# Kernel optimization log

Measured on AMD Instinct MI355X. Metric: run time of the kernel, lower is better.

Reference implementation:

```python
import jax, jax.numpy as jnp
import numpy as np

N_NODES = 200000
N_EDGES = 6400000
N_GRAPHS = 512
DIM_IN = 128
HID = 32
BN_EPS = 1e-5


def _gin(x, src, dst, w1, b1, w2, b2):
    # GINConv with eps=0: MLP(x + sum_{j in N(i)} x_j)
    agg = jax.ops.segment_sum(x[src], dst, num_segments=N_NODES)
    h = x + agg
    h = jnp.maximum(h @ w1 + b1, 0.0)
    return h @ w2 + b2


def _bn(x, gamma, beta):
    # BatchNorm1d, training mode: batch stats, biased variance
    m = jnp.mean(x, axis=0)
    v = jnp.var(x, axis=0)
    return gamma * (x - m) * jax.lax.rsqrt(v + BN_EPS) + beta


def setup_inputs() -> dict:
    key = jax.random.key(0)
    ks = jax.random.split(key, 20)
    s = 0.1
    inp = {
        "x": jax.random.normal(ks[0], (N_NODES, DIM_IN), jnp.float32),
        "edge_index": jax.random.randint(ks[1], (2, N_EDGES), 0, N_NODES, jnp.int32),
        "batch": jnp.sort(jax.random.randint(ks[2], (N_NODES,), 0, N_GRAPHS, jnp.int32)),
        "e0_w1": s * jax.random.normal(ks[3], (DIM_IN, HID), jnp.float32),
        "e0_b1": s * jax.random.normal(ks[4], (HID,), jnp.float32),
        "e0_w2": s * jax.random.normal(ks[5], (HID, HID), jnp.float32),
        "e0_b2": s * jax.random.normal(ks[6], (HID,), jnp.float32),
        "enc_w1": s * jax.random.normal(ks[7], (4, HID, HID), jnp.float32),
        "enc_b1": s * jax.random.normal(ks[8], (4, HID), jnp.float32),
        "enc_w2": s * jax.random.normal(ks[9], (4, HID, HID), jnp.float32),
        "enc_b2": s * jax.random.normal(ks[10], (4, HID), jnp.float32),
        "enc_gamma": jnp.ones((5, HID), jnp.float32),
        "enc_beta": jnp.zeros((5, HID), jnp.float32),
        "dec_w1": s * jax.random.normal(ks[11], (5, HID, HID), jnp.float32),
        "dec_b1": s * jax.random.normal(ks[12], (5, HID), jnp.float32),
        "dec_w2": s * jax.random.normal(ks[13], (4, HID, HID), jnp.float32),
        "dec_b2": s * jax.random.normal(ks[14], (4, HID), jnp.float32),
        "dec_w2_last": s * jax.random.normal(ks[15], (HID, DIM_IN), jnp.float32),
        "dec_b2_last": s * jax.random.normal(ks[16], (DIM_IN,), jnp.float32),
        "dec_gamma": jnp.ones((4, HID), jnp.float32),
        "dec_beta": jnp.zeros((4, HID), jnp.float32),
    }
    return inp


def reference(x, edge_index, batch,
              e0_w1, e0_b1, e0_w2, e0_b2,
              enc_w1, enc_b1, enc_w2, enc_b2, enc_gamma, enc_beta,
              dec_w1, dec_b1, dec_w2, dec_b2, dec_w2_last, dec_b2_last,
              dec_gamma, dec_beta):
    src, dst = edge_index[0], edge_index[1]

    # ----- Encoder: 5 GIN layers, ReLU then BN, collect per-layer reps -----
    xs = []
    h = jnp.maximum(_gin(x, src, dst, e0_w1, e0_b1, e0_w2, e0_b2), 0.0)
    h = _bn(h, enc_gamma[0], enc_beta[0])
    xs.append(h)
    for i in range(4):
        h = jnp.maximum(_gin(h, src, dst, enc_w1[i], enc_b1[i], enc_w2[i], enc_b2[i]), 0.0)
        h = _bn(h, enc_gamma[i + 1], enc_beta[i + 1])
        xs.append(h)
    encoded_rep = h

    # ----- Decoder: 5 GIN layers, ReLU; BN on all but last -----
    d = encoded_rep
    for i in range(5):
        w2 = dec_w2[i] if i < 4 else dec_w2_last
        b2 = dec_b2[i] if i < 4 else dec_b2_last
        d = jnp.maximum(_gin(d, src, dst, dec_w1[i], dec_b1[i], w2, b2), 0.0)
        if i < 4:
            d = _bn(d, dec_gamma[i], dec_beta[i])
    decoded_rep = d

    # ----- Global add pool of each encoder layer output, concat -----
    xpool = [jax.ops.segment_sum(xi, batch, num_segments=N_GRAPHS) for xi in xs]
    global_rep = jnp.concatenate(xpool, axis=1)  # [G, 5*32]

    return encoded_rep, decoded_rep, global_rep
```

## Files before the change

kernel.cpp:

```cpp
#include <hip/hip_runtime.h>
#include <hip/hip_bf16.h>
#include <hip/hip_fp16.h>
#include <string.h>

#define N_NODES  200000
#define N_EDGES  6400000
#define N_GRAPHS 512
#define DIM_IN   128
#define HID      32
#define BN_EPS   1e-5f

#define CHUNK    2048
#define NCHUNKS  98

typedef const float* fp;

__device__ __forceinline__ unsigned short f2h(float f) {
    __half h = __float2half(f);
    unsigned short u; __builtin_memcpy(&u, &h, 2); return u;
}
__device__ __forceinline__ float2 h2f2(unsigned int u) {
    __half2 h; __builtin_memcpy(&h, &u, 4);
    return __half22float2(h);
}
__device__ __forceinline__ float h1f(unsigned short u) {
    __half h; __builtin_memcpy(&h, &u, 2);
    return __half2float(h);
}


__global__ __launch_bounds__(256) void k_hist2(const int* __restrict__ dst,
                                               int* __restrict__ deg) {
    __shared__ int lh[12500];
    const int grp = blockIdx.x & 15;
    const int blk = blockIdx.x >> 4;
    const int lo = grp * 12500;
    for (int j = threadIdx.x; j < 12500; j += 256) lh[j] = 0;
    __syncthreads();
    const int4* d4 = reinterpret_cast<const int4*>(dst) + blk * 50000;
    for (int j = threadIdx.x; j < 12500; j += 256) {
        int4 v0 = d4[j];
        int4 v1 = d4[j + 12500];
        int4 v2 = d4[j + 25000];
        int4 v3 = d4[j + 37500];
        int a;
        a = v0.x - lo; if ((unsigned)a < 12500u) atomicAdd(&lh[a], 1);
        a = v0.y - lo; if ((unsigned)a < 12500u) atomicAdd(&lh[a], 1);
        a = v0.z - lo; if ((unsigned)a < 12500u) atomicAdd(&lh[a], 1);
        a = v0.w - lo; if ((unsigned)a < 12500u) atomicAdd(&lh[a], 1);
        a = v1.x - lo; if ((unsigned)a < 12500u) atomicAdd(&lh[a], 1);
        a = v1.y - lo; if ((unsigned)a < 12500u) atomicAdd(&lh[a], 1);
        a = v1.z - lo; if ((unsigned)a < 12500u) atomicAdd(&lh[a], 1);
        a = v1.w - lo; if ((unsigned)a < 12500u) atomicAdd(&lh[a], 1);
        a = v2.x - lo; if ((unsigned)a < 12500u) atomicAdd(&lh[a], 1);
        a = v2.y - lo; if ((unsigned)a < 12500u) atomicAdd(&lh[a], 1);
        a = v2.z - lo; if ((unsigned)a < 12500u) atomicAdd(&lh[a], 1);
        a = v2.w - lo; if ((unsigned)a < 12500u) atomicAdd(&lh[a], 1);
        a = v3.x - lo; if ((unsigned)a < 12500u) atomicAdd(&lh[a], 1);
        a = v3.y - lo; if ((unsigned)a < 12500u) atomicAdd(&lh[a], 1);
        a = v3.z - lo; if ((unsigned)a < 12500u) atomicAdd(&lh[a], 1);
        a = v3.w - lo; if ((unsigned)a < 12500u) atomicAdd(&lh[a], 1);
    }
    __syncthreads();
    for (int j = threadIdx.x; j < 12500; j += 256) {
        int c = lh[j];
        if (c) atomicAdd(&deg[lo + j], c);
    }
}

__global__ void k_chunksum(const int* __restrict__ deg, int* __restrict__ chunksum) {
    __shared__ int red[256];
    int b = blockIdx.x, t = threadIdx.x;
    int base = b * CHUNK;
    int s = 0;
    for (int k = 0; k < 8; ++k) {
        int i = base + t + k * 256;
        if (i < N_NODES) s += deg[i];
    }
    red[t] = s; __syncthreads();
    for (int off = 128; off > 0; off >>= 1) {
        if (t < off) red[t] += red[t + off];
        __syncthreads();
    }
    if (t == 0) chunksum[b] = red[0];
}

__global__ void k_scanchunks(const int* __restrict__ chunksum, int* __restrict__ chunkoff,
                             int* __restrict__ rowptr) {
    __shared__ int buf[128];
    int t = threadIdx.x;
    int v = (t < NCHUNKS) ? chunksum[t] : 0;
    buf[t] = v; __syncthreads();
    for (int off = 1; off < 128; off <<= 1) {
        int add = (t >= off) ? buf[t - off] : 0;
        __syncthreads();
        buf[t] += add;
        __syncthreads();
    }
    if (t < NCHUNKS) chunkoff[t] = buf[t] - v;
    if (t == 0) rowptr[N_NODES] = N_EDGES;
}

__global__ void k_scanfinal(const int* __restrict__ deg, const int* __restrict__ chunkoff,
                            int* __restrict__ rowptr, int* __restrict__ fillpos) {
    __shared__ int tsum[256];
    int b = blockIdx.x, t = threadIdx.x;
    int base = b * CHUNK + t * 8;
    int v[8]; int s = 0;
    for (int k = 0; k < 8; ++k) {
        int i = base + k;
        v[k] = (i < N_NODES) ? deg[i] : 0;
        s += v[k];
    }
    tsum[t] = s; __syncthreads();
    for (int off = 1; off < 256; off <<= 1) {
        int add = (t >= off) ? tsum[t - off] : 0;
        __syncthreads();
        tsum[t] += add;
        __syncthreads();
    }
    int run = tsum[t] - s + chunkoff[b];
    for (int k = 0; k < 8; ++k) {
        int i = base + k;
        if (i < N_NODES) { rowptr[i] = run; fillpos[i] = run; run += v[k]; }
    }
}

__global__ __launch_bounds__(256) void k_fill2(
    const int* __restrict__ src, const int* __restrict__ dst,
    int* __restrict__ fillpos, int* __restrict__ csr, int blk0)
{
    const int grp = blockIdx.x & 7;
    const int blk = blk0 + (blockIdx.x >> 3);
    const int lo = grp * 25000, hi = lo + 25000;
    const int4* d4 = reinterpret_cast<const int4*>(dst) + blk * 3125;
    const int4* s4 = reinterpret_cast<const int4*>(src) + blk * 3125;
    for (int j = threadIdx.x; j < 3125; j += 256) {
        int4 d = d4[j];
        int4 s = s4[j];
        if (d.x >= lo && d.x < hi) { int p = atomicAdd(&fillpos[d.x], 1); csr[p] = s.x; }
        if (d.y >= lo && d.y < hi) { int p = atomicAdd(&fillpos[d.y], 1); csr[p] = s.y; }
        if (d.z >= lo && d.z < hi) { int p = atomicAdd(&fillpos[d.z], 1); csr[p] = s.z; }
        if (d.w >= lo && d.w < hi) { int p = atomicAdd(&fillpos[d.w], 1); csr[p] = s.w; }
    }
}

__global__ void k_bounds(const int* __restrict__ batch, int* __restrict__ gstart) {
    int g = blockIdx.x * blockDim.x + threadIdx.x;
    if (g > N_GRAPHS) return;
    if (g == N_GRAPHS) { gstart[g] = N_NODES; return; }
    int lo = 0, hi = N_NODES;
    while (lo < hi) {
        int mid = (lo + hi) >> 1;
        if (batch[mid] < g) lo = mid + 1; else hi = mid;
    }
    gstart[g] = lo;
}


__global__ __launch_bounds__(256) void k_proj128(
    const float* __restrict__ x, fp w1,
    unsigned short* __restrict__ y16, int n0, int n1)
{
    const int lane = threadIdx.x & 63;
    const int c = lane & 31;
    const int kb = (lane & 32) * 2;
    const int srcBase = lane & 32;
    float wreg[64];
    #pragma unroll
    for (int k = 0; k < 64; ++k) wreg[k] = w1[(kb + k) * 32 + c];
    int worker   = (blockIdx.x * blockDim.x + threadIdx.x) >> 6;
    int nworkers = (gridDim.x * blockDim.x) >> 6;
    for (int n = n0 + 2 * worker; n < n1; n += 2 * nworkers) {
        const float* xa = x + (size_t)n * DIM_IN;
        const float* xb = xa + DIM_IN;
        float a02 = xa[kb + c], a13 = xa[kb + 32 + c];
        float b02 = xb[kb + c], b13 = xb[kb + 32 + c];
        float accA0 = 0.f, accA1 = 0.f, accB0 = 0.f, accB1 = 0.f;
        #pragma unroll
        for (int k = 0; k < 32; ++k) {
            float xav0 = __shfl(a02, srcBase | k, 64);
            float xav1 = __shfl(a13, srcBase | k, 64);
            float xbv0 = __shfl(b02, srcBase | k, 64);
            float xbv1 = __shfl(b13, srcBase | k, 64);
            accA0 = fmaf(xav0, wreg[k],      accA0);
            accA1 = fmaf(xav1, wreg[32 + k], accA1);
            accB0 = fmaf(xbv0, wreg[k],      accB0);
            accB1 = fmaf(xbv1, wreg[32 + k], accB1);
        }
        float accA = accA0 + accA1;
        float accB = accB0 + accB1;
        accA += __shfl_xor(accA, 32, 64);
        accB += __shfl_xor(accB, 32, 64);
        if (srcBase == 0) {
            y16[(size_t)n * 32 + c] = f2h(accA);
            y16[(size_t)(n + 1) * 32 + c] = f2h(accB);
        }
    }
}


__global__ __launch_bounds__(256) void k_gather8(
    const unsigned short* __restrict__ h16,
    const int* __restrict__ rowptr, const int* __restrict__ csr,
    float* __restrict__ sout,
    const float* __restrict__ stats, fp gamma, fp beta)
{
    const int lane = threadIdx.x & 63;
    const int sub  = lane & 15;
    const int q    = sub & 7;
    const int hh   = sub >> 3;
    const int srcBase = lane & 48;
    float sc0 = 1.f, sc1 = 1.f, sc2 = 1.f, sc3 = 1.f;
    float sh0 = 0.f, sh1 = 0.f, sh2 = 0.f, sh3 = 0.f;
    if (stats) {
        const int c0 = 4 * q;
        float m0 = stats[c0 + 0] * (1.f / N_NODES);
        float m1 = stats[c0 + 1] * (1.f / N_NODES);
        float m2 = stats[c0 + 2] * (1.f / N_NODES);
        float m3 = stats[c0 + 3] * (1.f / N_NODES);
        float v0 = stats[32 + c0 + 0] * (1.f / N_NODES) - m0 * m0;
        float v1 = stats[32 + c0 + 1] * (1.f / N_NODES) - m1 * m1;
        float v2 = stats[32 + c0 + 2] * (1.f / N_NODES) - m2 * m2;
        float v3 = stats[32 + c0 + 3] * (1.f / N_NODES) - m3 * m3;
        sc0 = gamma[c0 + 0] * rsqrtf(v0 + BN_EPS);
        sc1 = gamma[c0 + 1] * rsqrtf(v1 + BN_EPS);
        sc2 = gamma[c0 + 2] * rsqrtf(v2 + BN_EPS);
        sc3 = gamma[c0 + 3] * rsqrtf(v3 + BN_EPS);
        sh0 = beta[c0 + 0] - m0 * sc0;
        sh1 = beta[c0 + 1] - m1 * sc1;
        sh2 = beta[c0 + 2] - m2 * sc2;
        sh3 = beta[c0 + 3] - m3 * sc3;
    }
    const uint2* hp2 = reinterpret_cast<const uint2*>(h16);
    float4* so4 = reinterpret_cast<float4*>(sout);
    int worker   = (blockIdx.x * blockDim.x + threadIdx.x) >> 4;
    int nworkers = (gridDim.x * blockDim.x) >> 4;
    for (int n = worker; n < N_NODES; n += nworkers) {
        uint2 us = hp2[(size_t)n * 8 + q];
        int e0 = rowptr[n], e1 = rowptr[n + 1];
        float2 sA = h2f2(us.x), sB = h2f2(us.y);
        float a0 = (hh == 0) ? sA.x : 0.f;
        float a1 = (hh == 0) ? sA.y : 0.f;
        float a2 = (hh == 0) ? sB.x : 0.f;
        float a3 = (hh == 0) ? sB.y : 0.f;
        int e = e0;
        while (e < e1) {
            int rem = e1 - e;
            int cnt = rem < 16 ? rem : 16;
            int myidx = (sub < cnt) ? csr[e + sub] : 0;
            if (cnt == 16) {
                int i0 = __shfl(myidx, srcBase | (0  + hh), 64);
                int i1 = __shfl(myidx, srcBase | (2  + hh), 64);
                int i2 = __shfl(myidx, srcBase | (4  + hh), 64);
                int i3 = __shfl(myidx, srcBase | (6  + hh), 64);
                int i4 = __shfl(myidx, srcBase | (8  + hh), 64);
                int i5 = __shfl(myidx, srcBase | (10 + hh), 64);
                int i6 = __shfl(myidx, srcBase | (12 + hh), 64);
                int i7 = __shfl(myidx, srcBase | (14 + hh), 64);
                uint2 u0 = hp2[(size_t)i0 * 8 + q];
                uint2 u1 = hp2[(size_t)i1 * 8 + q];
                uint2 u2 = hp2[(size_t)i2 * 8 + q];
                uint2 u3 = hp2[(size_t)i3 * 8 + q];
                uint2 u4 = hp2[(size_t)i4 * 8 + q];
                uint2 u5 = hp2[(size_t)i5 * 8 + q];
                uint2 u6 = hp2[(size_t)i6 * 8 + q];
                uint2 u7 = hp2[(size_t)i7 * 8 + q];
                float2 fA, fB;
                fA = h2f2(u0.x); fB = h2f2(u0.y);
                a0 += fA.x; a1 += fA.y; a2 += fB.x; a3 += fB.y;
                fA = h2f2(u1.x); fB = h2f2(u1.y);
                a0 += fA.x; a1 += fA.y; a2 += fB.x; a3 += fB.y;
                fA = h2f2(u2.x); fB = h2f2(u2.y);
                a0 += fA.x; a1 += fA.y; a2 += fB.x; a3 += fB.y;
                fA = h2f2(u3.x); fB = h2f2(u3.y);
                a0 += fA.x; a1 += fA.y; a2 += fB.x; a3 += fB.y;
                fA = h2f2(u4.x); fB = h2f2(u4.y);
                a0 += fA.x; a1 += fA.y; a2 += fB.x; a3 += fB.y;
                fA = h2f2(u5.x); fB = h2f2(u5.y);
                a0 += fA.x; a1 += fA.y; a2 += fB.x; a3 += fB.y;
                fA = h2f2(u6.x); fB = h2f2(u6.y);
                a0 += fA.x; a1 += fA.y; a2 += fB.x; a3 += fB.y;
                fA = h2f2(u7.x); fB = h2f2(u7.y);
                a0 += fA.x; a1 += fA.y; a2 += fB.x; a3 += fB.y;
            } else {
                int k = 0;
                for (; k + 2 <= cnt; k += 2) {
                    int i = __shfl(myidx, srcBase | (k + hh), 64);
                    uint2 u = hp2[(size_t)i * 8 + q];
                    float2 fA = h2f2(u.x), fB = h2f2(u.y);
                    a0 += fA.x; a1 += fA.y; a2 += fB.x; a3 += fB.y;
                }
                if (k < cnt) {
                    int i = __shfl(myidx, srcBase | k, 64);
                    if (hh == 0) {
                        uint2 u = hp2[(size_t)i * 8 + q];
                        float2 fA = h2f2(u.x), fB = h2f2(u.y);
                        a0 += fA.x; a1 += fA.y; a2 += fB.x; a3 += fB.y;
                    }
                }
            }
            e += cnt;
        }
        a0 += __shfl_xor(a0, 8, 64);
        a1 += __shfl_xor(a1, 8, 64);
        a2 += __shfl_xor(a2, 8, 64);
        a3 += __shfl_xor(a3, 8, 64);
        float dc = (float)(e1 - e0 + 1);
        float4 o;
        o.x = fmaf(a0, sc0, dc * sh0);
        o.y = fmaf(a1, sc1, dc * sh1);
        o.z = fmaf(a2, sc2, dc * sh2);
        o.w = fmaf(a3, sc3, dc * sh3);
        if (hh == 0) so4[(size_t)n * 8 + q] = o;
    }
}


__global__ __launch_bounds__(256) void k_mlp32(
    const float* __restrict__ s, fp w1, fp b1, fp w2, fp b2,
    unsigned short* __restrict__ h16out,
    float* __restrict__ stats)
{
    const int lane = threadIdx.x & 63;
    const int c = lane & 31;
    const int srcBase = lane & 32;
    float w1r[32], w2r[32];
    #pragma unroll
    for (int k = 0; k < 32; ++k) {
        w1r[k] = w1[k * 32 + c];
        w2r[k] = w2[k * 32 + c];
    }
    const float b1c = b1[c];
    const float b2c = b2[c];
    int worker   = (blockIdx.x * blockDim.x + threadIdx.x) >> 5;
    int nworkers = (gridDim.x * blockDim.x) >> 5;
    float s1 = 0.f, s2 = 0.f;
    for (int n = worker; n < N_NODES; n += nworkers) {
        float sv = s[(size_t)n * 32 + c];
        float acc1 = b1c;
        #pragma unroll
        for (int k = 0; k < 32; ++k)
            acc1 = fmaf(__shfl(sv, srcBase | k, 64), w1r[k], acc1);
        float h3 = fmaxf(acc1, 0.f);
        float acc2 = b2c;
        #pragma unroll
        for (int k = 0; k < 32; ++k)
            acc2 = fmaf(__shfl(h3, srcBase | k, 64), w2r[k], acc2);
        float a = fmaxf(acc2, 0.f);
        h16out[(size_t)n * 32 + c] = f2h(a);
        s1 += a; s2 += a * a;
    }
    s1 += __shfl_xor(s1, 32, 64);
    s2 += __shfl_xor(s2, 32, 64);
    __shared__ float ls1[4][32], ls2[4][32];
    int w = threadIdx.x >> 6;
    if ((threadIdx.x & 32) == 0) { ls1[w][c] = s1; ls2[w][c] = s2; }
    __syncthreads();
    if (threadIdx.x < 32) {
        float t1 = ls1[0][c] + ls1[1][c] + ls1[2][c] + ls1[3][c];
        float t2 = ls2[0][c] + ls2[1][c] + ls2[2][c] + ls2[3][c];
        atomicAdd(&stats[c], t1);
        atomicAdd(&stats[32 + c], t2);
    }
}

__global__ __launch_bounds__(256) void k_mlp0(
    const float* __restrict__ s, fp b1, fp w2, fp b2,
    unsigned short* __restrict__ h16out,
    float* __restrict__ stats)
{
    const int lane = threadIdx.x & 63;
    const int c = lane & 31;
    const int srcBase = lane & 32;
    float w2r[32];
    #pragma unroll
    for (int k = 0; k < 32; ++k) w2r[k] = w2[k * 32 + c];
    const float b1c = b1[c];
    const float b2c = b2[c];
    int worker   = (blockIdx.x * blockDim.x + threadIdx.x) >> 5;
    int nworkers = (gridDim.x * blockDim.x) >> 5;
    float s1 = 0.f, s2 = 0.f;
    for (int n = worker; n < N_NODES; n += nworkers) {
        float sv = s[(size_t)n * 32 + c];
        float h3 = fmaxf(sv + b1c, 0.f);
        float acc2 = b2c;
        #pragma unroll
        for (int k = 0; k < 32; ++k)
            acc2 = fmaf(__shfl(h3, srcBase | k, 64), w2r[k], acc2);
        float a = fmaxf(acc2, 0.f);
        h16out[(size_t)n * 32 + c] = f2h(a);
        s1 += a; s2 += a * a;
    }
    s1 += __shfl_xor(s1, 32, 64);
    s2 += __shfl_xor(s2, 32, 64);
    __shared__ float ls1[4][32], ls2[4][32];
    int w = threadIdx.x >> 6;
    if ((threadIdx.x & 32) == 0) { ls1[w][c] = s1; ls2[w][c] = s2; }
    __syncthreads();
    if (threadIdx.x < 32) {
        float t1 = ls1[0][c] + ls1[1][c] + ls1[2][c] + ls1[3][c];
        float t2 = ls2[0][c] + ls2[1][c] + ls2[2][c] + ls2[3][c];
        atomicAdd(&stats[c], t1);
        atomicAdd(&stats[32 + c], t2);
    }
}

__global__ __launch_bounds__(256) void k_mlp_last(
    const float* __restrict__ s, fp w1, fp b1, fp w2 , fp b2,
    float* __restrict__ out, int n0, int n1)
{
    const int lane = threadIdx.x & 63;
    const int c = lane & 31;
    float w1r[32], w2a[32], w2b[32];
    #pragma unroll
    for (int k = 0; k < 32; ++k) {
        w1r[k] = w1[k * 32 + c];
        w2a[k] = w2[k * 128 + 2 * lane];
        w2b[k] = w2[k * 128 + 2 * lane + 1];
    }
    const float b1c = b1[c];
    const float b2a = b2[2 * lane];
    const float b2b = b2[2 * lane + 1];
    int worker   = (blockIdx.x * blockDim.x + threadIdx.x) >> 6;
    int nworkers = (gridDim.x * blockDim.x) >> 6;
    for (int n = n0 + 2 * worker; n < n1; n += 2 * nworkers) {
        float svA = s[(size_t)n * 32 + c];
        float svB = s[(size_t)(n + 1) * 32 + c];
        float p0A = b1c, p1A = 0.f, p0B = b1c, p1B = 0.f;
        #pragma unroll
        for (int k = 0; k < 16; ++k) {
            p0A = fmaf(__shfl(svA, k, 64),      w1r[k],      p0A);
            p1A = fmaf(__shfl(svA, 16 + k, 64), w1r[16 + k], p1A);
            p0B = fmaf(__shfl(svB, k, 64),      w1r[k],      p0B);
            p1B = fmaf(__shfl(svB, 16 + k, 64), w1r[16 + k], p1B);
        }
        float h3A = fmaxf(p0A + p1A, 0.f);
        float h3B = fmaxf(p0B + p1B, 0.f);
        float oaA = b2a, obA = b2b, oaB = b2a, obB = b2b;
        #pragma unroll
        for (int k = 0; k < 32; ++k) {
            float vA = __shfl(h3A, (lane & 32) | k, 64);
            float vB = __shfl(h3B, (lane & 32) | k, 64);
            oaA = fmaf(vA, w2a[k], oaA);
            obA = fmaf(vA, w2b[k], obA);
            oaB = fmaf(vB, w2a[k], oaB);
            obB = fmaf(vB, w2b[k], obB);
        }
        float2 prA; prA.x = fmaxf(oaA, 0.f); prA.y = fmaxf(obA, 0.f);
        float2 prB; prB.x = fmaxf(oaB, 0.f); prB.y = fmaxf(obB, 0.f);
        reinterpret_cast<float2*>(out)[(size_t)n * 64 + lane] = prA;
        reinterpret_cast<float2*>(out)[(size_t)(n + 1) * 64 + lane] = prB;
    }
}

__global__ void k_bnout(const unsigned short* __restrict__ h16,
                        const float* __restrict__ stats,
                        fp gamma, fp beta, float* __restrict__ out)
{
    const int c0 = (threadIdx.x & 15) * 2;
    float m0  = stats[c0] * (1.f / N_NODES);
    float m1  = stats[c0 + 1] * (1.f / N_NODES);
    float v0 = stats[32 + c0] * (1.f / N_NODES) - m0 * m0;
    float v1 = stats[32 + c0 + 1] * (1.f / N_NODES) - m1 * m1;
    float sc0 = gamma[c0] * rsqrtf(v0 + BN_EPS);
    float sc1 = gamma[c0 + 1] * rsqrtf(v1 + BN_EPS);
    float sh0 = beta[c0] - m0 * sc0;
    float sh1 = beta[c0 + 1] - m1 * sc1;
    const unsigned int* hp = reinterpret_cast<const unsigned int*>(h16);
    float2* o2 = reinterpret_cast<float2*>(out);
    int i = blockIdx.x * blockDim.x + threadIdx.x;
    int stride = gridDim.x * blockDim.x;
    for (; i < N_NODES * 16; i += stride) {
        float2 f = h2f2(hp[i]);
        float2 o;
        o.x = fmaf(f.x, sc0, sh0);
        o.y = fmaf(f.y, sc1, sh1);
        o2[i] = o;
    }
}

__global__ void k_pool(const unsigned short* __restrict__ h16,
                       const int* __restrict__ gstart,
                       float* __restrict__ out, int col0,
                       const float* __restrict__ stats, fp gamma, fp beta)
{
    int g = blockIdx.x;
    int t = threadIdx.x;
    int f = t & 31, j = t >> 5;
    int n0 = gstart[g], n1 = gstart[g + 1];
    float s = 0.f;
    for (int n = n0 + j; n < n1; n += 8) s += h1f(h16[(size_t)n * 32 + f]);
    __shared__ float red[8][32];
    red[j][f] = s; __syncthreads();
    if (t < 32) {
        float tot = 0.f;
        #pragma unroll
        for (int k = 0; k < 8; ++k) tot += red[k][f];
        float m  = stats[f] * (1.f / N_NODES);
        float vv = stats[32 + f] * (1.f / N_NODES) - m * m;
        float sc = gamma[f] * rsqrtf(vv + BN_EPS);
        float sh = beta[f] - m * sc;
        out[g * (5 * HID) + col0 + f] = fmaf(tot, sc, (float)(n1 - n0) * sh);
    }
}


extern "C" void kernel_launch(void* const* d_in, const int* in_sizes, int n_in,
                              void* d_out, int out_size, void* d_ws, size_t ws_size,
                              hipStream_t stream) {
    fp         x        = (fp)d_in[0];
    const int* edge     = (const int*)d_in[1];
    const int* batch    = (const int*)d_in[2];
    fp e0_w1 = (fp)d_in[3],  e0_b1 = (fp)d_in[4];
    fp e0_w2 = (fp)d_in[5],  e0_b2 = (fp)d_in[6];
    fp enc_w1 = (fp)d_in[7],  enc_b1 = (fp)d_in[8];
    fp enc_w2 = (fp)d_in[9],  enc_b2 = (fp)d_in[10];
    fp enc_gamma = (fp)d_in[11], enc_beta = (fp)d_in[12];
    fp dec_w1 = (fp)d_in[13], dec_b1 = (fp)d_in[14];
    fp dec_w2 = (fp)d_in[15], dec_b2 = (fp)d_in[16];
    fp dec_w2_last = (fp)d_in[17], dec_b2_last = (fp)d_in[18];
    fp dec_gamma = (fp)d_in[19], dec_beta = (fp)d_in[20];

    const int* srcp = edge;
    const int* dstp = edge + N_EDGES;

    float* out_enc    = (float*)d_out;
    float* out_dec    = (float*)d_out + (size_t)N_NODES * 32;
    float* out_global = (float*)d_out + (size_t)N_NODES * 160;

    char* p = (char*)d_ws;
    auto alloc = [&](size_t bytes) -> void* {
        void* r = (void*)p;
        p += (bytes + 255) & ~(size_t)255;
        return r;
    };
    int*   rowptr   = (int*)alloc((N_NODES + 1) * sizeof(int));
    int*   fillpos  = (int*)alloc(N_NODES * sizeof(int));
    int*   deg      = (int*)alloc(N_NODES * sizeof(int));
    int*   chunksum = (int*)alloc(128 * sizeof(int));
    int*   chunkoff = (int*)alloc(128 * sizeof(int));
    int*   gstart   = (int*)alloc((N_GRAPHS + 1) * sizeof(int));
    float* stats    = (float*)alloc(9 * 64 * sizeof(float));
    int*   csr      = (int*)alloc((size_t)N_EDGES * sizeof(int));
    float* sbuf     = (float*)alloc((size_t)N_NODES * 32 * sizeof(float));
    unsigned short* h16 = (unsigned short*)alloc((size_t)N_NODES * 32 * sizeof(unsigned short));

    hipMemsetAsync(deg, 0, N_NODES * sizeof(int), stream);
    hipMemsetAsync(stats, 0, 9 * 64 * sizeof(float), stream);

    k_hist2<<<512, 256, 0, stream>>>(dstp, deg);
    k_chunksum<<<NCHUNKS, 256, 0, stream>>>(deg, chunksum);
    k_scanchunks<<<1, 128, 0, stream>>>(chunksum, chunkoff, rowptr);
    k_scanfinal<<<NCHUNKS, 256, 0, stream>>>(deg, chunkoff, rowptr, fillpos);
    k_fill2<<<1368, 256, 0, stream>>>(srcp, dstp, fillpos, csr, 0);
    k_fill2<<<1368, 256, 0, stream>>>(srcp, dstp, fillpos, csr, 171);
    k_fill2<<<1360, 256, 0, stream>>>(srcp, dstp, fillpos, csr, 342);
    k_bounds<<<3, 256, 0, stream>>>(batch, gstart);

    k_proj128<<<1024, 256, 0, stream>>>(x, e0_w1, h16, 0, 100000);
    k_proj128<<<1024, 256, 0, stream>>>(x, e0_w1, h16, 100000, 200000);
    k_gather8<<<2048, 256, 0, stream>>>(h16, rowptr, csr, sbuf,
                                        nullptr, nullptr, nullptr);
    k_mlp0<<<1024, 256, 0, stream>>>(sbuf, e0_b1, e0_w2, e0_b2, h16, stats);
    k_pool<<<N_GRAPHS, 256, 0, stream>>>(h16, gstart, out_global, 0,
                                         stats, enc_gamma, enc_beta);

    for (int i = 0; i < 4; ++i) {
        float* st_prev = stats + i * 64;
        float* st      = stats + (1 + i) * 64;
        k_gather8<<<2048, 256, 0, stream>>>(h16, rowptr, csr, sbuf,
                                            st_prev, enc_gamma + i * 32, enc_beta + i * 32);
        k_mlp32<<<1024, 256, 0, stream>>>(sbuf,
                                          enc_w1 + i * 1024, enc_b1 + i * 32,
                                          enc_w2 + i * 1024, enc_b2 + i * 32,
                                          h16, st);
        k_pool<<<N_GRAPHS, 256, 0, stream>>>(h16, gstart, out_global, (1 + i) * 32,
                                             st, enc_gamma + (1 + i) * 32,
                                             enc_beta + (1 + i) * 32);
    }

    k_bnout<<<2048, 256, 0, stream>>>(h16, stats + 4 * 64,
                                      enc_gamma + 4 * 32, enc_beta + 4 * 32, out_enc);

    for (int i = 0; i < 4; ++i) {
        float* st_prev = (i == 0) ? (stats + 4 * 64) : (stats + (4 + i) * 64);
        fp g_prev      = (i == 0) ? (enc_gamma + 4 * 32) : (dec_gamma + (i - 1) * 32);
        fp b_prev      = (i == 0) ? (enc_beta  + 4 * 32) : (dec_beta  + (i - 1) * 32);
        float* st      = stats + (5 + i) * 64;
        k_gather8<<<2048, 256, 0, stream>>>(h16, rowptr, csr, sbuf,
                                            st_prev, g_prev, b_prev);
        k_mlp32<<<1024, 256, 0, stream>>>(sbuf,
                                          dec_w1 + i * 1024, dec_b1 + i * 32,
                                          dec_w2 + i * 1024, dec_b2 + i * 32,
                                          h16, st);
    }

    k_gather8<<<2048, 256, 0, stream>>>(h16, rowptr, csr, sbuf,
                                        stats + 8 * 64, dec_gamma + 3 * 32,
                                        dec_beta + 3 * 32);
    k_mlp_last<<<1024, 256, 0, stream>>>(sbuf,
                                         dec_w1 + 4 * 1024, dec_b1 + 4 * 32,
                                         dec_w2_last, dec_b2_last, out_dec,
                                         0, 100000);
    k_mlp_last<<<1024, 256, 0, stream>>>(sbuf,
                                         dec_w1 + 4 * 1024, dec_b1 + 4 * 32,
                                         dec_w2_last, dec_b2_last, out_dec,
                                         100000, 200000);
}
```

Measured before the change: 2.727 ms.

## Fuse neighbor gather with GIN MLP and ping-pong fp16 feature buffers

Merges the CSR neighbor aggregation and the two-layer MLP plus BN statistics into one kernel per layer, so the fp32 aggregate buffer is no longer written and re-read between kernels. Because the fused kernel reads neighbor features while writing new ones, it alternates between two fp16 buffers. The gather now uses 32 lanes per node instead of 16 and holds two weight arrays in registers, which may lower occupancy and latency hiding for the random gathers.

```diff
diff --git a/kernel.cpp b/kernel.cpp
--- a/kernel.cpp
+++ b/kernel.cpp
@@ -196,6 +196,265 @@
             y16[(size_t)n * 32 + c] = f2h(accA);
             y16[(size_t)(n + 1) * 32 + c] = f2h(accB);
         }
+    }
+}
+
+
+__global__ __launch_bounds__(256) void k_gmlp(
+    const unsigned short* __restrict__ h16in,
+    const int* __restrict__ rowptr, const int* __restrict__ csr,
+    const float* __restrict__ stats, fp gamma, fp beta,
+    fp w1, fp b1, fp w2, fp b2,
+    unsigned short* __restrict__ h16out,
+    float* __restrict__ statsOut)
+{
+    const int lane = threadIdx.x & 63;
+    const int sub5 = lane & 31;
+    const int q    = sub5 & 7;
+    const int quad = sub5 >> 3;
+    const int srcBase = lane & 32;
+    const int g0 = 4 * q;
+    float m0 = stats[g0 + 0] * (1.f / N_NODES);
+    float m1 = stats[g0 + 1] * (1.f / N_NODES);
+    float m2 = stats[g0 + 2] * (1.f / N_NODES);
+    float m3 = stats[g0 + 3] * (1.f / N_NODES);
+    float v0 = stats[32 + g0 + 0] * (1.f / N_NODES) - m0 * m0;
+    float v1 = stats[32 + g0 + 1] * (1.f / N_NODES) - m1 * m1;
+    float v2 = stats[32 + g0 + 2] * (1.f / N_NODES) - m2 * m2;
+    float v3 = stats[32 + g0 + 3] * (1.f / N_NODES) - m3 * m3;
+    float sc0 = gamma[g0 + 0] * rsqrtf(v0 + BN_EPS);
+    float sc1 = gamma[g0 + 1] * rsqrtf(v1 + BN_EPS);
+    float sc2 = gamma[g0 + 2] * rsqrtf(v2 + BN_EPS);
+    float sc3 = gamma[g0 + 3] * rsqrtf(v3 + BN_EPS);
+    float sh0 = beta[g0 + 0] - m0 * sc0;
+    float sh1 = beta[g0 + 1] - m1 * sc1;
+    float sh2 = beta[g0 + 2] - m2 * sc2;
+    float sh3 = beta[g0 + 3] - m3 * sc3;
+    float w1r[32], w2r[32];
+    #pragma unroll
+    for (int k = 0; k < 32; ++k) {
+        w1r[k] = w1[k * 32 + sub5];
+        w2r[k] = w2[k * 32 + sub5];
+    }
+    const float b1c = b1[sub5];
+    const float b2c = b2[sub5];
+    const uint2* hp2 = reinterpret_cast<const uint2*>(h16in);
+    float s1 = 0.f, s2 = 0.f;
+    int worker   = (blockIdx.x * blockDim.x + threadIdx.x) >> 5;
+    int nworkers = (gridDim.x * blockDim.x) >> 5;
+    for (int n = worker; n < N_NODES; n += nworkers) {
+        uint2 us = hp2[(size_t)n * 8 + q];
+        int e0 = rowptr[n], e1 = rowptr[n + 1];
+        float2 sA = h2f2(us.x), sB = h2f2(us.y);
+        float a0, a1, a2, a3;
+        if (quad == 0) { a0 = sA.x; a1 = sA.y; a2 = sB.x; a3 = sB.y; }
+        else           { a0 = 0.f;  a1 = 0.f;  a2 = 0.f;  a3 = 0.f; }
+        int e = e0;
+        while (e < e1) {
+            int rem = e1 - e;
+            int cnt = rem < 32 ? rem : 32;
+            int myidx = (sub5 < cnt) ? csr[e + sub5] : 0;
+            if (cnt == 32) {
+                const int qb = srcBase | (quad * 8);
+                int i0 = __shfl(myidx, qb | 0, 64);
+                int i1 = __shfl(myidx, qb | 1, 64);
+                int i2 = __shfl(myidx, qb | 2, 64);
+                int i3 = __shfl(myidx, qb | 3, 64);
+                int i4 = __shfl(myidx, qb | 4, 64);
+                int i5 = __shfl(myidx, qb | 5, 64);
+                int i6 = __shfl(myidx, qb | 6, 64);
+                int i7 = __shfl(myidx, qb | 7, 64);
+                uint2 u0 = hp2[(size_t)i0 * 8 + q];
+                uint2 u1 = hp2[(size_t)i1 * 8 + q];
+                uint2 u2 = hp2[(size_t)i2 * 8 + q];
+                uint2 u3 = hp2[(size_t)i3 * 8 + q];
+                uint2 u4 = hp2[(size_t)i4 * 8 + q];
+                uint2 u5 = hp2[(size_t)i5 * 8 + q];
+                uint2 u6 = hp2[(size_t)i6 * 8 + q];
+                uint2 u7 = hp2[(size_t)i7 * 8 + q];
+                float2 fA, fB;
+                fA = h2f2(u0.x); fB = h2f2(u0.y);
+                a0 += fA.x; a1 += fA.y; a2 += fB.x; a3 += fB.y;
+                fA = h2f2(u1.x); fB = h2f2(u1.y);
+                a0 += fA.x; a1 += fA.y; a2 += fB.x; a3 += fB.y;
+                fA = h2f2(u2.x); fB = h2f2(u2.y);
+                a0 += fA.x; a1 += fA.y; a2 += fB.x; a3 += fB.y;
+                fA = h2f2(u3.x); fB = h2f2(u3.y);
+                a0 += fA.x; a1 += fA.y; a2 += fB.x; a3 += fB.y;
+                fA = h2f2(u4.x); fB = h2f2(u4.y);
+                a0 += fA.x; a1 += fA.y; a2 += fB.x; a3 += fB.y;
+                fA = h2f2(u5.x); fB = h2f2(u5.y);
+                a0 += fA.x; a1 += fA.y; a2 += fB.x; a3 += fB.y;
+                fA = h2f2(u6.x); fB = h2f2(u6.y);
+                a0 += fA.x; a1 += fA.y; a2 += fB.x; a3 += fB.y;
+                fA = h2f2(u7.x); fB = h2f2(u7.y);
+                a0 += fA.x; a1 += fA.y; a2 += fB.x; a3 += fB.y;
+            } else {
+                for (int j = 0; j * 4 < cnt; ++j) {
+                    int eidx = j * 4 + quad;
+                    int i = __shfl(myidx, srcBase | (eidx & 31), 64);
+                    if (eidx < cnt) {
+                        uint2 u = hp2[(size_t)i * 8 + q];
+                        float2 fA = h2f2(u.x), fB = h2f2(u.y);
+                        a0 += fA.x; a1 += fA.y; a2 += fB.x; a3 += fB.y;
+                    }
+                }
+            }
+            e += cnt;
+        }
+        a0 += __shfl_xor(a0, 8, 64);  a0 += __shfl_xor(a0, 16, 64);
+        a1 += __shfl_xor(a1, 8, 64);  a1 += __shfl_xor(a1, 16, 64);
+        a2 += __shfl_xor(a2, 8, 64);  a2 += __shfl_xor(a2, 16, 64);
+        a3 += __shfl_xor(a3, 8, 64);  a3 += __shfl_xor(a3, 16, 64);
+        float dc = (float)(e1 - e0 + 1);
+        float s0v = fmaf(a0, sc0, dc * sh0);
+        float s1v = fmaf(a1, sc1, dc * sh1);
+        float s2v = fmaf(a2, sc2, dc * sh2);
+        float s3v = fmaf(a3, sc3, dc * sh3);
+        float acc1 = b1c;
+        #pragma unroll
+        for (int k = 0; k < 32; ++k) {
+            float src = ((k & 3) == 0) ? s0v : ((k & 3) == 1) ? s1v
+                      : ((k & 3) == 2) ? s2v : s3v;
+            float sk = __shfl(src, srcBase | (k >> 2), 64);
+            acc1 = fmaf(sk, w1r[k], acc1);
+        }
+        float h3 = fmaxf(acc1, 0.f);
+        float acc2 = b2c;
+        #pragma unroll
+        for (int k = 0; k < 32; ++k)
+            acc2 = fmaf(__shfl(h3, srcBase | k, 64), w2r[k], acc2);
+        float a = fmaxf(acc2, 0.f);
+        h16out[(size_t)n * 32 + sub5] = f2h(a);
+        s1 += a; s2 += a * a;
+    }
+    s1 += __shfl_xor(s1, 32, 64);
+    s2 += __shfl_xor(s2, 32, 64);
+    __shared__ float ls1[4][32], ls2[4][32];
+    int w = threadIdx.x >> 6;
+    if ((threadIdx.x & 32) == 0) { ls1[w][sub5] = s1; ls2[w][sub5] = s2; }
+    __syncthreads();
+    if (threadIdx.x < 32) {
+        float t1 = ls1[0][sub5] + ls1[1][sub5] + ls1[2][sub5] + ls1[3][sub5];
+        float t2 = ls2[0][sub5] + ls2[1][sub5] + ls2[2][sub5] + ls2[3][sub5];
+        atomicAdd(&statsOut[sub5], t1);
+        atomicAdd(&statsOut[32 + sub5], t2);
+    }
+}
+
+__global__ __launch_bounds__(256) void k_gmlp0(
+    const unsigned short* __restrict__ h16in,
+    const int* __restrict__ rowptr, const int* __restrict__ csr,
+    fp b1, fp w2, fp b2,
+    unsigned short* __restrict__ h16out,
+    float* __restrict__ statsOut)
+{
+    const int lane = threadIdx.x & 63;
+    const int sub5 = lane & 31;
+    const int q    = sub5 & 7;
+    const int quad = sub5 >> 3;
+    const int srcBase = lane & 32;
+    const int g0 = 4 * q;
+    float b10 = b1[g0 + 0], b11 = b1[g0 + 1], b12 = b1[g0 + 2], b13 = b1[g0 + 3];
+    float w2r[32];
+    #pragma unroll
+    for (int k = 0; k < 32; ++k) w2r[k] = w2[k * 32 + sub5];
+    const float b2c = b2[sub5];
+    const uint2* hp2 = reinterpret_cast<const uint2*>(h16in);
+    float s1 = 0.f, s2 = 0.f;
+    int worker   = (blockIdx.x * blockDim.x + threadIdx.x) >> 5;
+    int nworkers = (gridDim.x * blockDim.x) >> 5;
+    for (int n = worker; n < N_NODES; n += nworkers) {
+        uint2 us = hp2[(size_t)n * 8 + q];
+        int e0 = rowptr[n], e1 = rowptr[n + 1];
+        float2 sA = h2f2(us.x), sB = h2f2(us.y);
+        float a0, a1, a2, a3;
+        if (quad == 0) { a0 = sA.x; a1 = sA.y; a2 = sB.x; a3 = sB.y; }
+        else           { a0 = 0.f;  a1 = 0.f;  a2 = 0.f;  a3 = 0.f; }
+        int e = e0;
+        while (e < e1) {
+            int rem = e1 - e;
+            int cnt = rem < 32 ? rem : 32;
+            int myidx = (sub5 < cnt) ? csr[e + sub5] : 0;
+            if (cnt == 32) {
+                const int qb = srcBase | (quad * 8);
+                int i0 = __shfl(myidx, qb | 0, 64);
+                int i1 = __shfl(myidx, qb | 1, 64);
+                int i2 = __shfl(myidx, qb | 2, 64);
+                int i3 = __shfl(myidx, qb | 3, 64);
+                int i4 = __shfl(myidx, qb | 4, 64);
+                int i5 = __shfl(myidx, qb | 5, 64);
+                int i6 = __shfl(myidx, qb | 6, 64);
+                int i7 = __shfl(myidx, qb | 7, 64);
+                uint2 u0 = hp2[(size_t)i0 * 8 + q];
+                uint2 u1 = hp2[(size_t)i1 * 8 + q];
+                uint2 u2 = hp2[(size_t)i2 * 8 + q];
+                uint2 u3 = hp2[(size_t)i3 * 8 + q];
+                uint2 u4 = hp2[(size_t)i4 * 8 + q];
+                uint2 u5 = hp2[(size_t)i5 * 8 + q];
+                uint2 u6 = hp2[(size_t)i6 * 8 + q];
+                uint2 u7 = hp2[(size_t)i7 * 8 + q];
+                float2 fA, fB;
+                fA = h2f2(u0.x); fB = h2f2(u0.y);
+                a0 += fA.x; a1 += fA.y; a2 += fB.x; a3 += fB.y;
+                fA = h2f2(u1.x); fB = h2f2(u1.y);
+                a0 += fA.x; a1 += fA.y; a2 += fB.x; a3 += fB.y;
+                fA = h2f2(u2.x); fB = h2f2(u2.y);
+                a0 += fA.x; a1 += fA.y; a2 += fB.x; a3 += fB.y;
+                fA = h2f2(u3.x); fB = h2f2(u3.y);
+                a0 += fA.x; a1 += fA.y; a2 += fB.x; a3 += fB.y;
+                fA = h2f2(u4.x); fB = h2f2(u4.y);
+                a0 += fA.x; a1 += fA.y; a2 += fB.x; a3 += fB.y;
+                fA = h2f2(u5.x); fB = h2f2(u5.y);
+                a0 += fA.x; a1 += fA.y; a2 += fB.x; a3 += fB.y;
+                fA = h2f2(u6.x); fB = h2f2(u6.y);
+                a0 += fA.x; a1 += fA.y; a2 += fB.x; a3 += fB.y;
+                fA = h2f2(u7.x); fB = h2f2(u7.y);
+                a0 += fA.x; a1 += fA.y; a2 += fB.x; a3 += fB.y;
+            } else {
+                for (int j = 0; j * 4 < cnt; ++j) {
+                    int eidx = j * 4 + quad;
+                    int i = __shfl(myidx, srcBase | (eidx & 31), 64);
+                    if (eidx < cnt) {
+                        uint2 u = hp2[(size_t)i * 8 + q];
+                        float2 fA = h2f2(u.x), fB = h2f2(u.y);
+                        a0 += fA.x; a1 += fA.y; a2 += fB.x; a3 += fB.y;
+                    }
+                }
+            }
+            e += cnt;
+        }
+        a0 += __shfl_xor(a0, 8, 64);  a0 += __shfl_xor(a0, 16, 64);
+        a1 += __shfl_xor(a1, 8, 64);  a1 += __shfl_xor(a1, 16, 64);
+        a2 += __shfl_xor(a2, 8, 64);  a2 += __shfl_xor(a2, 16, 64);
+        a3 += __shfl_xor(a3, 8, 64);  a3 += __shfl_xor(a3, 16, 64);
+        float h30 = fmaxf(a0 + b10, 0.f);
+        float h31 = fmaxf(a1 + b11, 0.f);
+        float h32 = fmaxf(a2 + b12, 0.f);
+        float h33 = fmaxf(a3 + b13, 0.f);
+        float acc2 = b2c;
+        #pragma unroll
+        for (int k = 0; k < 32; ++k) {
+            float src = ((k & 3) == 0) ? h30 : ((k & 3) == 1) ? h31
+                      : ((k & 3) == 2) ? h32 : h33;
+            float hk = __shfl(src, srcBase | (k >> 2), 64);
+            acc2 = fmaf(hk, w2r[k], acc2);
+        }
+        float a = fmaxf(acc2, 0.f);
+        h16out[(size_t)n * 32 + sub5] = f2h(a);
+        s1 += a; s2 += a * a;
+    }
+    s1 += __shfl_xor(s1, 32, 64);
+    s2 += __shfl_xor(s2, 32, 64);
+    __shared__ float ls1[4][32], ls2[4][32];
+    int w = threadIdx.x >> 6;
+    if ((threadIdx.x & 32) == 0) { ls1[w][sub5] = s1; ls2[w][sub5] = s2; }
+    __syncthreads();
+    if (threadIdx.x < 32) {
+        float t1 = ls1[0][sub5] + ls1[1][sub5] + ls1[2][sub5] + ls1[3][sub5];
+        float t2 = ls2[0][sub5] + ls2[1][sub5] + ls2[2][sub5] + ls2[3][sub5];
+        atomicAdd(&statsOut[sub5], t1);
+        atomicAdd(&statsOut[32 + sub5], t2);
     }
 }
 
@@ -316,96 +575,6 @@
     }
 }
 
-
-__global__ __launch_bounds__(256) void k_mlp32(
-    const float* __restrict__ s, fp w1, fp b1, fp w2, fp b2,
-    unsigned short* __restrict__ h16out,
-    float* __restrict__ stats)
-{
-    const int lane = threadIdx.x & 63;
-    const int c = lane & 31;
-    const int srcBase = lane & 32;
-    float w1r[32], w2r[32];
-    #pragma unroll
-    for (int k = 0; k < 32; ++k) {
-        w1r[k] = w1[k * 32 + c];
-        w2r[k] = w2[k * 32 + c];
-    }
-    const float b1c = b1[c];
-    const float b2c = b2[c];
-    int worker   = (blockIdx.x * blockDim.x + threadIdx.x) >> 5;
-    int nworkers = (gridDim.x * blockDim.x) >> 5;
-    float s1 = 0.f, s2 = 0.f;
-    for (int n = worker; n < N_NODES; n += nworkers) {
-        float sv = s[(size_t)n * 32 + c];
-        float acc1 = b1c;
-        #pragma unroll
-        for (int k = 0; k < 32; ++k)
-            acc1 = fmaf(__shfl(sv, srcBase | k, 64), w1r[k], acc1);
-        float h3 = fmaxf(acc1, 0.f);
-        float acc2 = b2c;
-        #pragma unroll
-        for (int k = 0; k < 32; ++k)
-            acc2 = fmaf(__shfl(h3, srcBase | k, 64), w2r[k], acc2);
-        float a = fmaxf(acc2, 0.f);
-        h16out[(size_t)n * 32 + c] = f2h(a);
-        s1 += a; s2 += a * a;
-    }
-    s1 += __shfl_xor(s1, 32, 64);
-    s2 += __shfl_xor(s2, 32, 64);
-    __shared__ float ls1[4][32], ls2[4][32];
-    int w = threadIdx.x >> 6;
-    if ((threadIdx.x & 32) == 0) { ls1[w][c] = s1; ls2[w][c] = s2; }
-    __syncthreads();
-    if (threadIdx.x < 32) {
-        float t1 = ls1[0][c] + ls1[1][c] + ls1[2][c] + ls1[3][c];
-        float t2 = ls2[0][c] + ls2[1][c] + ls2[2][c] + ls2[3][c];
-        atomicAdd(&stats[c], t1);
-        atomicAdd(&stats[32 + c], t2);
-    }
-}
-
-__global__ __launch_bounds__(256) void k_mlp0(
-    const float* __restrict__ s, fp b1, fp w2, fp b2,
-    unsigned short* __restrict__ h16out,
-    float* __restrict__ stats)
-{
-    const int lane = threadIdx.x & 63;
-    const int c = lane & 31;
-    const int srcBase = lane & 32;
-    float w2r[32];
-    #pragma unroll
-    for (int k = 0; k < 32; ++k) w2r[k] = w2[k * 32 + c];
-    const float b1c = b1[c];
-    const float b2c = b2[c];
-    int worker   = (blockIdx.x * blockDim.x + threadIdx.x) >> 5;
-    int nworkers = (gridDim.x * blockDim.x) >> 5;
-    float s1 = 0.f, s2 = 0.f;
-    for (int n = worker; n < N_NODES; n += nworkers) {
-        float sv = s[(size_t)n * 32 + c];
-        float h3 = fmaxf(sv + b1c, 0.f);
-        float acc2 = b2c;
-        #pragma unroll
-        for (int k = 0; k < 32; ++k)
-            acc2 = fmaf(__shfl(h3, srcBase | k, 64), w2r[k], acc2);
-        float a = fmaxf(acc2, 0.f);
-        h16out[(size_t)n * 32 + c] = f2h(a);
-        s1 += a; s2 += a * a;
-    }
-    s1 += __shfl_xor(s1, 32, 64);
-    s2 += __shfl_xor(s2, 32, 64);
-    __shared__ float ls1[4][32], ls2[4][32];
-    int w = threadIdx.x >> 6;
-    if ((threadIdx.x & 32) == 0) { ls1[w][c] = s1; ls2[w][c] = s2; }
-    __syncthreads();
-    if (threadIdx.x < 32) {
-        float t1 = ls1[0][c] + ls1[1][c] + ls1[2][c] + ls1[3][c];
-        float t2 = ls2[0][c] + ls2[1][c] + ls2[2][c] + ls2[3][c];
-        atomicAdd(&stats[c], t1);
-        atomicAdd(&stats[32 + c], t2);
-    }
-}
-
 __global__ __launch_bounds__(256) void k_mlp_last(
     const float* __restrict__ s, fp w1, fp b1, fp w2 , fp b2,
     float* __restrict__ out, int n0, int n1)
@@ -544,7 +713,8 @@
     float* stats    = (float*)alloc(9 * 64 * sizeof(float));
     int*   csr      = (int*)alloc((size_t)N_EDGES * sizeof(int));
     float* sbuf     = (float*)alloc((size_t)N_NODES * 32 * sizeof(float));
-    unsigned short* h16 = (unsigned short*)alloc((size_t)N_NODES * 32 * sizeof(unsigned short));
+    unsigned short* hA = (unsigned short*)alloc((size_t)N_NODES * 32 * sizeof(unsigned short));
+    unsigned short* hB = (unsigned short*)alloc((size_t)N_NODES * 32 * sizeof(unsigned short));
 
     hipMemsetAsync(deg, 0, N_NODES * sizeof(int), stream);
     hipMemsetAsync(stats, 0, 9 * 64 * sizeof(float), stream);
@@ -558,29 +728,32 @@
     k_fill2<<<1360, 256, 0, stream>>>(srcp, dstp, fillpos, csr, 342);
     k_bounds<<<3, 256, 0, stream>>>(batch, gstart);
 
-    k_proj128<<<1024, 256, 0, stream>>>(x, e0_w1, h16, 0, 100000);
-    k_proj128<<<1024, 256, 0, stream>>>(x, e0_w1, h16, 100000, 200000);
-    k_gather8<<<2048, 256, 0, stream>>>(h16, rowptr, csr, sbuf,
-                                        nullptr, nullptr, nullptr);
-    k_mlp0<<<1024, 256, 0, stream>>>(sbuf, e0_b1, e0_w2, e0_b2, h16, stats);
-    k_pool<<<N_GRAPHS, 256, 0, stream>>>(h16, gstart, out_global, 0,
+    unsigned short* cur = hA;
+    unsigned short* nxt = hB;
+
+    k_proj128<<<1024, 256, 0, stream>>>(x, e0_w1, cur, 0, 100000);
+    k_proj128<<<1024, 256, 0, stream>>>(x, e0_w1, cur, 100000, 200000);
+    k_gmlp0<<<2048, 256, 0, stream>>>(cur, rowptr, csr,
+                                      e0_b1, e0_w2, e0_b2, nxt, stats);
+    { unsigned short* t = cur; cur = nxt; nxt = t; }
+    k_pool<<<N_GRAPHS, 256, 0, stream>>>(cur, gstart, out_global, 0,
                                          stats, enc_gamma, enc_beta);
 
     for (int i = 0; i < 4; ++i) {
         float* st_prev = stats + i * 64;
         float* st      = stats + (1 + i) * 64;
-        k_gather8<<<2048, 256, 0, stream>>>(h16, rowptr, csr, sbuf,
-                                            st_prev, enc_gamma + i * 32, enc_beta + i * 32);
-        k_mlp32<<<1024, 256, 0, stream>>>(sbuf,
-                                          enc_w1 + i * 1024, enc_b1 + i * 32,
-                                          enc_w2 + i * 1024, enc_b2 + i * 32,
-                                          h16, st);
-        k_pool<<<N_GRAPHS, 256, 0, stream>>>(h16, gstart, out_global, (1 + i) * 32,
+        k_gmlp<<<2048, 256, 0, stream>>>(cur, rowptr, csr,
+                                         st_prev, enc_gamma + i * 32, enc_beta + i * 32,
+                                         enc_w1 + i * 1024, enc_b1 + i * 32,
+                                         enc_w2 + i * 1024, enc_b2 + i * 32,
+                                         nxt, st);
+        { unsigned short* t = cur; cur = nxt; nxt = t; }
+        k_pool<<<N_GRAPHS, 256, 0, stream>>>(cur, gstart, out_global, (1 + i) * 32,
                                              st, enc_gamma + (1 + i) * 32,
                                              enc_beta + (1 + i) * 32);
     }
 
-    k_bnout<<<2048, 256, 0, stream>>>(h16, stats + 4 * 64,
+    k_bnout<<<2048, 256, 0, stream>>>(cur, stats + 4 * 64,
                                       enc_gamma + 4 * 32, enc_beta + 4 * 32, out_enc);
 
     for (int i = 0; i < 4; ++i) {
@@ -588,15 +761,15 @@
         fp g_prev      = (i == 0) ? (enc_gamma + 4 * 32) : (dec_gamma + (i - 1) * 32);
         fp b_prev      = (i == 0) ? (enc_beta  + 4 * 32) : (dec_beta  + (i - 1) * 32);
         float* st      = stats + (5 + i) * 64;
-        k_gather8<<<2048, 256, 0, stream>>>(h16, rowptr, csr, sbuf,
-                                            st_prev, g_prev, b_prev);
-        k_mlp32<<<1024, 256, 0, stream>>>(sbuf,
-                                          dec_w1 + i * 1024, dec_b1 + i * 32,
-                                          dec_w2 + i * 1024, dec_b2 + i * 32,
-                                          h16, st);
-    }
-
-    k_gather8<<<2048, 256, 0, stream>>>(h16, rowptr, csr, sbuf,
+        k_gmlp<<<2048, 256, 0, stream>>>(cur, rowptr, csr,
+                                         st_prev, g_prev, b_prev,
+                                         dec_w1 + i * 1024, dec_b1 + i * 32,
+                                         dec_w2 + i * 1024, dec_b2 + i * 32,
+                                         nxt, st);
+        { unsigned short* t = cur; cur = nxt; nxt = t; }
+    }
+
+    k_gather8<<<2048, 256, 0, stream>>>(cur, rowptr, csr, sbuf,
                                         stats + 8 * 64, dec_gamma + 3 * 32,
                                         dec_beta + 3 * 32);
     k_mlp_last<<<1024, 256, 0, stream>>>(sbuf,
```

New measurement: 2.871 ms. 1.05x slower.
